# Kernel optimization log

Measured on AMD Instinct MI355X. Metric: run time of the kernel, lower is better.

## Reference

```python
import jax, jax.numpy as jnp
import numpy as np

N = 100000   # nodes
E = 3200000  # edges per graph
D = 16       # embedding_size, num_heads = 1
ATTN_SLOPE = 0.2   # DGL GATv2Conv negative_slope default
ACT_SLOPE = 0.01   # torch.nn.functional.leaky_relu default (activation arg)


def gatv2_layer(h, src, dst, W_src, b_src, W_dst, b_dst, attn):
    """DGL GATv2Conv with num_heads=1, activation=leaky_relu.
    h: [N, D]; src/dst: [E] int; W_*: [D, D]; b_*: [D]; attn: [D].
    """
    feat_src = h @ W_src + b_src          # [N, D]
    feat_dst = h @ W_dst + b_dst          # [N, D]
    el = feat_src[src]                    # [E, D] gather to edges
    e = jax.nn.leaky_relu(el + feat_dst[dst], ATTN_SLOPE)  # [E, D]
    score = e @ attn                      # [E] attention logits
    # segment softmax over incoming edges of each destination node
    smax = jax.ops.segment_max(score, dst, num_segments=N)
    smax = jnp.where(jnp.isfinite(smax), smax, 0.0)  # empty segments -> 0
    ex = jnp.exp(score - smax[dst])       # [E]
    denom = jax.ops.segment_sum(ex, dst, num_segments=N)  # [N]
    alpha = ex / denom[dst]               # [E]
    rst = jax.ops.segment_sum(alpha[:, None] * el, dst, num_segments=N)  # [N, D]
    return jax.nn.leaky_relu(rst, ACT_SLOPE)


def setup_inputs() -> dict:
    key = jax.random.key(0)
    ks = jax.random.split(key, 16)
    s = 1.0 / np.sqrt(D)
    return {
        "embedding": jax.random.normal(ks[0], (N, D), jnp.float32),
        "src1": jax.random.randint(ks[1], (E,), 0, N, jnp.int32),
        "dst1": jax.random.randint(ks[2], (E,), 0, N, jnp.int32),
        "src2": jax.random.randint(ks[3], (E,), 0, N, jnp.int32),
        "dst2": jax.random.randint(ks[4], (E,), 0, N, jnp.int32),
        "W_src1": jax.random.normal(ks[5], (D, D), jnp.float32) * s,
        "b_src1": jnp.zeros((D,), jnp.float32),
        "W_dst1": jax.random.normal(ks[6], (D, D), jnp.float32) * s,
        "b_dst1": jnp.zeros((D,), jnp.float32),
        "attn1": jax.random.normal(ks[7], (D,), jnp.float32) * s,
        "W_src2": jax.random.normal(ks[8], (D, D), jnp.float32) * s,
        "b_src2": jnp.zeros((D,), jnp.float32),
        "W_dst2": jax.random.normal(ks[9], (D, D), jnp.float32) * s,
        "b_dst2": jnp.zeros((D,), jnp.float32),
        "attn2": jax.random.normal(ks[10], (D,), jnp.float32) * s,
    }


def reference(embedding, src1, dst1, src2, dst2,
              W_src1, b_src1, W_dst1, b_dst1, attn1,
              W_src2, b_src2, W_dst2, b_dst2, attn2):
    user2item = gatv2_layer(embedding, src1, dst1, W_src1, b_src1, W_dst1, b_dst1, attn1)
    item_influence = gatv2_layer(user2item, src2, dst2, W_src2, b_src2, W_dst2, b_dst2, attn2)
    return item_influence  # [N, D]
```

## Files before the change

kernel.cpp:

```cpp
#include <hip/hip_runtime.h>
#include <hip/hip_fp16.h>

#define D 16
#define R 64
#define RBITS 6
#define RMASK 63
#define STRIDE 2560
#define CAP 2560
#define KPT (CAP / 256)
#define EPB 8192
#define SBT 1024
#define NBMAX 2048
#define ATTN_SLOPE 0.2f
#define ACT_SLOPE 0.01f

__device__ __forceinline__ float leaky_a(float v) {
    return v > 0.f ? v : ATTN_SLOPE * v;
}

__device__ __forceinline__ float2 h2f(unsigned u) {
    __half2 h = *(__half2*)&u;
    return __half22float2(h);
}

__device__ __forceinline__ int block_scan_pair(int pair, int tid, int* swsum) {
    int lane = tid & 63, w = tid >> 6;
    int x = pair;
#pragma unroll
    for (int ofs = 1; ofs < 64; ofs <<= 1) {
        int y = __shfl_up(x, ofs, 64);
        if (lane >= ofs) x += y;
    }
    if (lane == 63) swsum[w] = x;
    __syncthreads();
    if (w == 0) {
        int v = (lane < 16) ? swsum[lane] : 0;
        int s = v;
#pragma unroll
        for (int ofs = 1; ofs < 16; ofs <<= 1) {
            int y = __shfl_up(s, ofs, 64);
            if (lane >= ofs) s += y;
        }
        if (lane < 16) swsum[lane] = s - v;
    }
    __syncthreads();
    return x - pair + swsum[w];
}

__global__ void node_transform_kernel(const float* __restrict__ h,
                                      const float* __restrict__ Wsrc,
                                      const float* __restrict__ bsrc,
                                      const float* __restrict__ Wdst,
                                      const float* __restrict__ bdst,
                                      __half* __restrict__ feat_src_h,
                                      float* __restrict__ feat_dst,
                                      int* __restrict__ gcur,
                                      int N, int NB) {
    __shared__ float sWs[D * D], sWd[D * D], sbs[D], sbd[D];
    int t = threadIdx.x;
    if (t < D * D) {
        sWs[t] = Wsrc[t];
        sWd[t] = Wdst[t];
    }
    if (t < D) {
        sbs[t] = bsrc[t];
        sbd[t] = bdst[t];
    }
    int n = blockIdx.x * blockDim.x + t;
    if (n < NB) gcur[n] = n * STRIDE;
    __syncthreads();
    if (n >= N) return;
    float hv[D];
    const float4* h4 = (const float4*)(h + (size_t)n * D);
#pragma unroll
    for (int k = 0; k < 4; k++) {
        float4 v = h4[k];
        hv[4 * k] = v.x; hv[4 * k + 1] = v.y; hv[4 * k + 2] = v.z; hv[4 * k + 3] = v.w;
    }
    float os[D], od[D];
#pragma unroll
    for (int d = 0; d < D; d++) {
        float ss = sbs[d];
        float sd = sbd[d];
#pragma unroll
        for (int k = 0; k < D; k++) {
            ss += hv[k] * sWs[k * D + d];
            sd += hv[k] * sWd[k * D + d];
        }
        os[d] = ss; od[d] = sd;
    }
    unsigned us[8];
#pragma unroll
    for (int k = 0; k < 8; k++) {
        __half2 hh = __floats2half2_rn(os[2 * k], os[2 * k + 1]);
        us[k] = *(unsigned*)&hh;
    }
    uint4* fo = (uint4*)(feat_src_h + (size_t)n * D);
    fo[0] = make_uint4(us[0], us[1], us[2], us[3]);
    fo[1] = make_uint4(us[4], us[5], us[6], us[7]);
    float4* fd4 = (float4*)(feat_dst + (size_t)n * D);
#pragma unroll
    for (int k = 0; k < 4; k++)
        fd4[k] = make_float4(od[4 * k], od[4 * k + 1], od[4 * k + 2], od[4 * k + 3]);
}

__global__ void binscatter_kernel(const int* __restrict__ src, const int* __restrict__ dst,
                                  int* __restrict__ gcur, unsigned* __restrict__ binned,
                                  int E, int NB) {
    __shared__ unsigned sorted[EPB];
    __shared__ unsigned short sposb[EPB];
    __shared__ int shist[NBMAX];
    __shared__ int soffs[NBMAX];
    __shared__ int sgbase[NBMAX];
    __shared__ int swsum[16];
    int tid = threadIdx.x;
    int base = blockIdx.x * EPB;
    int count = E - base;
    if (count > EPB) count = EPB;

    for (int i = tid; i < NB; i += SBT) shist[i] = 0;
    __syncthreads();
    if (base + EPB <= E) {
        const int4* d4 = (const int4*)(dst + base);
#pragma unroll
        for (int k = 0; k < EPB / SBT / 4; k++) {
            int4 v = d4[k * SBT + tid];
            atomicAdd(&shist[v.x >> RBITS], 1);
            atomicAdd(&shist[v.y >> RBITS], 1);
            atomicAdd(&shist[v.z >> RBITS], 1);
            atomicAdd(&shist[v.w >> RBITS], 1);
        }
    } else {
#pragma unroll
        for (int k = 0; k < EPB / SBT; k++) {
            int e = base + k * SBT + tid;
            if (e < E) atomicAdd(&shist[dst[e] >> RBITS], 1);
        }
    }
    __syncthreads();
    int i0 = 2 * tid, i1 = 2 * tid + 1;
    int a0 = (i0 < NB) ? shist[i0] : 0;
    int a1 = (i1 < NB) ? shist[i1] : 0;
    int excl = block_scan_pair(a0 + a1, tid, swsum);
    if (i0 < NB) {
        shist[i0] = excl;
        soffs[i0] = excl;
        if (a0 > 0) sgbase[i0] = atomicAdd(&gcur[i0], a0);
    }
    if (i1 < NB) {
        shist[i1] = excl + a0;
        soffs[i1] = excl + a0;
        if (a1 > 0) sgbase[i1] = atomicAdd(&gcur[i1], a1);
    }
    __syncthreads();
    if (base + EPB <= E) {
        const int4* s4 = (const int4*)(src + base);
        const int4* d4 = (const int4*)(dst + base);
#pragma unroll
        for (int k = 0; k < EPB / SBT / 4; k++) {
            int4 sv = s4[k * SBT + tid];
            int4 dv = d4[k * SBT + tid];
            int ss[4] = {sv.x, sv.y, sv.z, sv.w};
            int dd[4] = {dv.x, dv.y, dv.z, dv.w};
#pragma unroll
            for (int m = 0; m < 4; m++) {
                int b = dd[m] >> RBITS;
                int r = atomicAdd(&soffs[b], 1);
                sorted[r] = ((unsigned)ss[m] << RBITS) | (unsigned)(dd[m] & RMASK);
                sposb[r] = (unsigned short)b;
            }
        }
    } else {
#pragma unroll
        for (int k = 0; k < EPB / SBT; k++) {
            int e = base + k * SBT + tid;
            if (e < E) {
                int dv = dst[e];
                int b = dv >> RBITS;
                int r = atomicAdd(&soffs[b], 1);
                sorted[r] = ((unsigned)src[e] << RBITS) | (unsigned)(dv & RMASK);
                sposb[r] = (unsigned short)b;
            }
        }
    }
    __syncthreads();
#pragma unroll
    for (int k = 0; k < EPB / SBT; k++) {
        int p = k * SBT + tid;
        if (p < count) {
            int bb = sposb[p];
            int pos = sgbase[bb] + (p - shist[bb]);
            if (pos < (bb + 1) * STRIDE) binned[pos] = sorted[p];
        }
    }
}

__global__ void __launch_bounds__(256)
accumulate_kernel(const unsigned* __restrict__ binned,
                  const int* __restrict__ gcur,
                  const __half* __restrict__ feat_src_h,
                  const float* __restrict__ feat_dst,
                  const float* __restrict__ attn,
                  float* __restrict__ out, int N) {
    __shared__ float sfd[R * D];
    __shared__ int ebuf[CAP];
    __shared__ float exbuf[CAP];
    __shared__ int cstart[R + 1];
    __shared__ int cur[R];
    int b = blockIdx.x;
    int tid = threadIdx.x;
    int node0 = b * R;
    int nn = N - node0;
    if (nn > R) nn = R;
    for (int i = tid; i < nn * D; i += 256) sfd[i] = feat_dst[node0 * D + i];
    if (tid <= R) cstart[tid] = 0;

    float av[D];
#pragma unroll
    for (int k = 0; k < D; k++) av[k] = attn[k];

    int base = b * STRIDE;
    int cnt = gcur[b] - base;
    if (cnt > CAP) cnt = CAP;

    unsigned pls[KPT];
#pragma unroll
    for (int k = 0; k < KPT; k++) {
        int j = k * 256 + tid;
        pls[k] = (j < cnt) ? binned[base + j] : 0xFFFFFFFFu;
    }
    __syncthreads();

    const uint4* fsh4 = (const uint4*)feat_src_h;
    const uint2* fsq = (const uint2*)feat_src_h;
    const float4* sfd4 = (const float4*)sfd;

#pragma unroll
    for (int k = 0; k < KPT; k++)
        if (pls[k] != 0xFFFFFFFFu) atomicAdd(&cstart[pls[k] & RMASK], 1);

    float exs[KPT];
#pragma unroll
    for (int k = 0; k < KPT; k += 2) {
        unsigned q0 = pls[k], q1 = pls[k + 1];
        uint4 ua0, ub0, ua1, ub1;
        if (q0 != 0xFFFFFFFFu) {
            int s = q0 >> RBITS;
            ua0 = fsh4[2 * s]; ub0 = fsh4[2 * s + 1];
        }
        if (q1 != 0xFFFFFFFFu) {
            int s = q1 >> RBITS;
            ua1 = fsh4[2 * s]; ub1 = fsh4[2 * s + 1];
        }
        if (q0 != 0xFFFFFFFFu) {
            int loc = q0 & RMASK;
            float4 f0 = sfd4[loc * 4 + 0], f1 = sfd4[loc * 4 + 1];
            float4 f2 = sfd4[loc * 4 + 2], f3 = sfd4[loc * 4 + 3];
            float2 c0 = h2f(ua0.x), c1 = h2f(ua0.y), c2 = h2f(ua0.z), c3 = h2f(ua0.w);
            float2 c4 = h2f(ub0.x), c5 = h2f(ub0.y), c6 = h2f(ub0.z), c7 = h2f(ub0.w);
            float p = leaky_a(c0.x + f0.x) * av[0]  + leaky_a(c0.y + f0.y) * av[1]
                    + leaky_a(c1.x + f0.z) * av[2]  + leaky_a(c1.y + f0.w) * av[3]
                    + leaky_a(c2.x + f1.x) * av[4]  + leaky_a(c2.y + f1.y) * av[5]
                    + leaky_a(c3.x + f1.z) * av[6]  + leaky_a(c3.y + f1.w) * av[7]
                    + leaky_a(c4.x + f2.x) * av[8]  + leaky_a(c4.y + f2.y) * av[9]
                    + leaky_a(c5.x + f2.z) * av[10] + leaky_a(c5.y + f2.w) * av[11]
                    + leaky_a(c6.x + f3.x) * av[12] + leaky_a(c6.y + f3.y) * av[13]
                    + leaky_a(c7.x + f3.z) * av[14] + leaky_a(c7.y + f3.w) * av[15];
            exs[k] = __expf(p);
        }
        if (q1 != 0xFFFFFFFFu) {
            int loc = q1 & RMASK;
            float4 f0 = sfd4[loc * 4 + 0], f1 = sfd4[loc * 4 + 1];
            float4 f2 = sfd4[loc * 4 + 2], f3 = sfd4[loc * 4 + 3];
            float2 c0 = h2f(ua1.x), c1 = h2f(ua1.y), c2 = h2f(ua1.z), c3 = h2f(ua1.w);
            float2 c4 = h2f(ub1.x), c5 = h2f(ub1.y), c6 = h2f(ub1.z), c7 = h2f(ub1.w);
            float p = leaky_a(c0.x + f0.x) * av[0]  + leaky_a(c0.y + f0.y) * av[1]
                    + leaky_a(c1.x + f0.z) * av[2]  + leaky_a(c1.y + f0.w) * av[3]
                    + leaky_a(c2.x + f1.x) * av[4]  + leaky_a(c2.y + f1.y) * av[5]
                    + leaky_a(c3.x + f1.z) * av[6]  + leaky_a(c3.y + f1.w) * av[7]
                    + leaky_a(c4.x + f2.x) * av[8]  + leaky_a(c4.y + f2.y) * av[9]
                    + leaky_a(c5.x + f2.z) * av[10] + leaky_a(c5.y + f2.w) * av[11]
                    + leaky_a(c6.x + f3.x) * av[12] + leaky_a(c6.y + f3.y) * av[13]
                    + leaky_a(c7.x + f3.z) * av[14] + leaky_a(c7.y + f3.w) * av[15];
            exs[k + 1] = __expf(p);
        }
    }
    __syncthreads();
    if (tid < R) {
        int v = cstart[tid];
        int x = v;
#pragma unroll
        for (int ofs = 1; ofs < 64; ofs <<= 1) {
            int y = __shfl_up(x, ofs, 64);
            if (tid >= ofs) x += y;
        }
        cstart[tid] = x - v;
        cur[tid] = x - v;
        if (tid == R - 1) cstart[R] = x;
    }
    __syncthreads();
#pragma unroll
    for (int k = 0; k < KPT; k++) {
        unsigned pl = pls[k];
        if (pl != 0xFFFFFFFFu) {
            int r = atomicAdd(&cur[pl & RMASK], 1);
            ebuf[r] = (int)pl;
            exbuf[r] = exs[k];
        }
    }
    __syncthreads();

    int lane = tid & 63;
    int w = tid >> 6;
    int q = lane & 3;
    int s2 = (lane >> 2) & 3;
    int n2 = lane >> 4;

    float4 acc[4];
    float den[4];
#pragma unroll
    for (int i = 0; i < 4; i++) {
        acc[i] = make_float4(0.f, 0.f, 0.f, 0.f);
        den[i] = 0.f;
    }
#pragma unroll
    for (int i = 0; i < 4; i++) {
        int loc = w * 16 + i * 4 + n2;
        int kb = cstart[loc], ke = cstart[loc + 1];
        int k = kb + s2;
        for (; k + 12 < ke; k += 16) {
            int pl0 = ebuf[k];
            int pl1 = ebuf[k + 4];
            int pl2 = ebuf[k + 8];
            int pl3 = ebuf[k + 12];
            float ex0 = exbuf[k];
            float ex1 = exbuf[k + 4];
            float ex2 = exbuf[k + 8];
            float ex3 = exbuf[k + 12];
            uint2 u0 = fsq[(((unsigned)pl0) >> RBITS) * 4 + q];
            uint2 u1 = fsq[(((unsigned)pl1) >> RBITS) * 4 + q];
            uint2 u2 = fsq[(((unsigned)pl2) >> RBITS) * 4 + q];
            uint2 u3 = fsq[(((unsigned)pl3) >> RBITS) * 4 + q];
            float2 a01 = h2f(u0.x), a23 = h2f(u0.y);
            float2 b01 = h2f(u1.x), b23 = h2f(u1.y);
            float2 c01 = h2f(u2.x), c23 = h2f(u2.y);
            float2 d01 = h2f(u3.x), d23 = h2f(u3.y);
            acc[i].x += ex0 * a01.x + ex1 * b01.x + ex2 * c01.x + ex3 * d01.x;
            acc[i].y += ex0 * a01.y + ex1 * b01.y + ex2 * c01.y + ex3 * d01.y;
            acc[i].z += ex0 * a23.x + ex1 * b23.x + ex2 * c23.x + ex3 * d23.x;
            acc[i].w += ex0 * a23.y + ex1 * b23.y + ex2 * c23.y + ex3 * d23.y;
            den[i] += (ex0 + ex1) + (ex2 + ex3);
        }
        for (; k < ke; k += 4) {
            int pl = ebuf[k];
            float ex = exbuf[k];
            uint2 u = fsq[(((unsigned)pl) >> RBITS) * 4 + q];
            float2 a01 = h2f(u.x), a23 = h2f(u.y);
            acc[i].x += ex * a01.x;
            acc[i].y += ex * a01.y;
            acc[i].z += ex * a23.x;
            acc[i].w += ex * a23.y;
            den[i] += ex;
        }
    }
#pragma unroll
    for (int i = 0; i < 4; i++) {
        float4 a = acc[i];
        float dn = den[i];
#pragma unroll
        for (int m = 4; m <= 8; m <<= 1) {
            a.x += __shfl_xor(a.x, m, 16);
            a.y += __shfl_xor(a.y, m, 16);
            a.z += __shfl_xor(a.z, m, 16);
            a.w += __shfl_xor(a.w, m, 16);
            dn += __shfl_xor(dn, m, 16);
        }
        int loc = w * 16 + i * 4 + n2;
        if (s2 == 0 && loc < nn) {
            float inv = dn > 0.f ? 1.f / dn : 0.f;
            float4 v;
            v.x = a.x * inv; v.x = v.x > 0.f ? v.x : ACT_SLOPE * v.x;
            v.y = a.y * inv; v.y = v.y > 0.f ? v.y : ACT_SLOPE * v.y;
            v.z = a.z * inv; v.z = v.z > 0.f ? v.z : ACT_SLOPE * v.z;
            v.w = a.w * inv; v.w = v.w > 0.f ? v.w : ACT_SLOPE * v.w;
            ((float4*)out)[(size_t)(node0 + loc) * 4 + q] = v;
        }
    }
}

static void run_layer(const float* h, const int* src, const int* dst,
                      const float* Wsrc, const float* bsrc,
                      const float* Wdst, const float* bdst, const float* attn,
                      __half* feat_src_h, float* feat_dst,
                      int* gcur, unsigned* binned,
                      float* out, int N, int E, hipStream_t stream) {
    const int NB = (N + R - 1) / R;
    const int EB = (E + EPB - 1) / EPB;

    node_transform_kernel<<<(N + 255) / 256, 256, 0, stream>>>(
        h, Wsrc, bsrc, Wdst, bdst, feat_src_h, feat_dst, gcur, N, NB);

    binscatter_kernel<<<EB, SBT, 0, stream>>>(src, dst, gcur, binned, E, NB);

    accumulate_kernel<<<NB, 256, 0, stream>>>(
        binned, gcur, feat_src_h, feat_dst, attn, out, N);
}

extern "C" void kernel_launch(void* const* d_in, const int* in_sizes, int n_in,
                              void* d_out, int out_size, void* d_ws, size_t ws_size,
                              hipStream_t stream) {
    const float* emb = (const float*)d_in[0];
    const int* src1 = (const int*)d_in[1];
    const int* dst1 = (const int*)d_in[2];
    const int* src2 = (const int*)d_in[3];
    const int* dst2 = (const int*)d_in[4];
    const float* Wsrc1 = (const float*)d_in[5];
    const float* bsrc1 = (const float*)d_in[6];
    const float* Wdst1 = (const float*)d_in[7];
    const float* bdst1 = (const float*)d_in[8];
    const float* attn1 = (const float*)d_in[9];
    const float* Wsrc2 = (const float*)d_in[10];
    const float* bsrc2 = (const float*)d_in[11];
    const float* Wdst2 = (const float*)d_in[12];
    const float* bdst2 = (const float*)d_in[13];
    const float* attn2 = (const float*)d_in[14];

    const int N = in_sizes[0] / D;
    const int E1 = in_sizes[1];
    const int E2 = in_sizes[3];

    float* ws = (float*)d_ws;
    float* feat_dst = ws;
    float* h2 = feat_dst + (size_t)N * D;
    __half* feat_src_h = (__half*)(h2 + (size_t)N * D);
    int* gcur = (int*)(feat_src_h + (size_t)N * D);
    unsigned* binned = (unsigned*)(gcur + NBMAX);
    (void)ws_size; (void)n_in; (void)out_size;

    run_layer(emb, src1, dst1, Wsrc1, bsrc1, Wdst1, bdst1, attn1,
              feat_src_h, feat_dst, gcur, binned, h2, N, E1, stream);

    run_layer(h2, src2, dst2, Wsrc2, bsrc2, Wdst2, bdst2, attn2,
              feat_src_h, feat_dst, gcur, binned, (float*)d_out, N, E2, stream);
}
```

Measured before the change: 275.4 us.

## Fuse both GATv2 layers into one persistent cooperative kernel with grid syncs

```diff
diff --git a/kernel.cpp b/kernel.cpp
--- a/kernel.cpp
+++ b/kernel.cpp
@@ -1,5 +1,8 @@
 #include <hip/hip_runtime.h>
 #include <hip/hip_fp16.h>
+#include <hip/hip_cooperative_groups.h>
+
+namespace cg = cooperative_groups;
 
 #define D 16
 #define R 64
@@ -8,19 +11,445 @@
 #define STRIDE 2560
 #define CAP 2560
 #define KPT (CAP / 256)
+#define ATTN_SLOPE 0.2f
+#define ACT_SLOPE 0.01f
+
+#define EPB2 2048
+#define NBX 1600
+#define SBUF_BYTES 25152
+#define NUM_CU 256
+
 #define EPB 8192
 #define SBT 1024
 #define NBMAX 2048
-#define ATTN_SLOPE 0.2f
-#define ACT_SLOPE 0.01f
 
 __device__ __forceinline__ float leaky_a(float v) {
     return v > 0.f ? v : ATTN_SLOPE * v;
 }
-
 __device__ __forceinline__ float2 h2f(unsigned u) {
     __half2 h = *(__half2*)&u;
     return __half22float2(h);
+}
+
+
+struct FusedParams {
+    const float* emb;
+    const int *src1, *dst1, *src2, *dst2;
+    const float *Ws1, *bs1, *Wd1, *bd1, *at1;
+    const float *Ws2, *bs2, *Wd2, *bd2, *at2;
+    __half* fs1h; float* fd1;
+    __half* fs2h; float* fd2;
+    int* gA; int* gB;
+    unsigned* binned;
+    float* out;
+    int N, E1, E2, NB;
+};
+
+__device__ void transform_phase(const float* __restrict__ h,
+                                const float* __restrict__ Ws, const float* __restrict__ bs,
+                                const float* __restrict__ Wd, const float* __restrict__ bd,
+                                __half* __restrict__ fsh, float* __restrict__ fdst,
+                                int* __restrict__ gA, int* __restrict__ gB,
+                                int N, int NB, char* sbuf, int gtid, int gsize) {
+    float* wb = (float*)sbuf;
+    int tid = threadIdx.x;
+    wb[tid] = Ws[tid];
+    wb[256 + tid] = Wd[tid];
+    if (tid < 16) { wb[512 + tid] = bs[tid]; wb[528 + tid] = bd[tid]; }
+    __syncthreads();
+    for (int i = gtid; i < NB; i += gsize) { gA[i] = 0; gB[i] = 0; }
+    for (int n = gtid; n < N; n += gsize) {
+        const float4* h4 = (const float4*)(h + (size_t)n * D);
+        float hv[16];
+#pragma unroll
+        for (int k2 = 0; k2 < 4; k2++) {
+            float4 v = h4[k2];
+            hv[4 * k2] = v.x; hv[4 * k2 + 1] = v.y; hv[4 * k2 + 2] = v.z; hv[4 * k2 + 3] = v.w;
+        }
+        uint2* fo = (uint2*)(fsh + (size_t)n * D);
+        float4* fdo = (float4*)(fdst + (size_t)n * D);
+#pragma unroll
+        for (int q = 0; q < 4; q++) {
+            float s0 = wb[512 + 4 * q], s1 = wb[513 + 4 * q], s2 = wb[514 + 4 * q], s3 = wb[515 + 4 * q];
+            float d0 = wb[528 + 4 * q], d1 = wb[529 + 4 * q], d2 = wb[530 + 4 * q], d3 = wb[531 + 4 * q];
+#pragma unroll
+            for (int k = 0; k < 16; k++) {
+                float hk = hv[k];
+                const float* wr = &wb[k * 16 + 4 * q];
+                const float* wr2 = &wb[256 + k * 16 + 4 * q];
+                s0 += hk * wr[0]; s1 += hk * wr[1]; s2 += hk * wr[2]; s3 += hk * wr[3];
+                d0 += hk * wr2[0]; d1 += hk * wr2[1]; d2 += hk * wr2[2]; d3 += hk * wr2[3];
+            }
+            __half2 p0 = __floats2half2_rn(s0, s1), p1 = __floats2half2_rn(s2, s3);
+            fo[q] = make_uint2(*(unsigned*)&p0, *(unsigned*)&p1);
+            fdo[q] = make_float4(d0, d1, d2, d3);
+        }
+    }
+}
+
+__device__ void binscatter_phase(const int* __restrict__ src, const int* __restrict__ dst,
+                                 int* __restrict__ gcur, unsigned* __restrict__ binned,
+                                 int E, int NB, char* sbuf) {
+    unsigned* sorted = (unsigned*)sbuf;
+    unsigned short* sposb = (unsigned short*)(sbuf + 8192);
+    int* soffs = (int*)(sbuf + 12288);
+    int* delta = (int*)(sbuf + 12288 + 4 * NBX);
+    int* wsum = (int*)(sbuf + 12288 + 8 * NBX);
+    int tid = threadIdx.x;
+    int numTiles = (E + EPB2 - 1) / EPB2;
+    for (int tile = blockIdx.x; tile < numTiles; tile += gridDim.x) {
+        __syncthreads();
+        int base = tile * EPB2;
+        int count = E - base;
+        if (count > EPB2) count = EPB2;
+        for (int i = tid; i < NB; i += 256) soffs[i] = 0;
+        __syncthreads();
+        if (count == EPB2) {
+            const int4* d4 = (const int4*)(dst + base);
+            int4 a = d4[tid], b = d4[256 + tid];
+            atomicAdd(&soffs[a.x >> RBITS], 1); atomicAdd(&soffs[a.y >> RBITS], 1);
+            atomicAdd(&soffs[a.z >> RBITS], 1); atomicAdd(&soffs[a.w >> RBITS], 1);
+            atomicAdd(&soffs[b.x >> RBITS], 1); atomicAdd(&soffs[b.y >> RBITS], 1);
+            atomicAdd(&soffs[b.z >> RBITS], 1); atomicAdd(&soffs[b.w >> RBITS], 1);
+        } else {
+            for (int k = 0; k < 8; k++) {
+                int e = base + k * 256 + tid;
+                if (e < E) atomicAdd(&soffs[dst[e] >> RBITS], 1);
+            }
+        }
+        __syncthreads();
+        int c[8];
+        int tsum = 0;
+#pragma unroll
+        for (int m = 0; m < 8; m++) {
+            int i = tid * 8 + m;
+            c[m] = (i < NB) ? soffs[i] : 0;
+            tsum += c[m];
+        }
+        int lane = tid & 63, w = tid >> 6;
+        int x = tsum;
+#pragma unroll
+        for (int ofs = 1; ofs < 64; ofs <<= 1) {
+            int y = __shfl_up(x, ofs, 64);
+            if (lane >= ofs) x += y;
+        }
+        if (lane == 63) wsum[w] = x;
+        __syncthreads();
+        int wofs = 0;
+        if (w > 0) wofs += wsum[0];
+        if (w > 1) wofs += wsum[1];
+        if (w > 2) wofs += wsum[2];
+        int run = x - tsum + wofs;
+        __syncthreads();
+#pragma unroll
+        for (int m = 0; m < 8; m++) {
+            int i = tid * 8 + m;
+            if (i < NB) {
+                soffs[i] = run;
+                if (c[m] > 0) {
+                    int res = atomicAdd(&gcur[i], c[m]);
+                    delta[i] = i * STRIDE + res - run;
+                }
+                run += c[m];
+            }
+        }
+        __syncthreads();
+        if (count == EPB2) {
+            const int4* s4 = (const int4*)(src + base);
+            const int4* d4 = (const int4*)(dst + base);
+            int4 sa = s4[tid], sb = s4[256 + tid], da = d4[tid], db = d4[256 + tid];
+            int ssv[8] = {sa.x, sa.y, sa.z, sa.w, sb.x, sb.y, sb.z, sb.w};
+            int ddv[8] = {da.x, da.y, da.z, da.w, db.x, db.y, db.z, db.w};
+#pragma unroll
+            for (int m = 0; m < 8; m++) {
+                int b = ddv[m] >> RBITS;
+                int r = atomicAdd(&soffs[b], 1);
+                sorted[r] = ((unsigned)ssv[m] << RBITS) | (unsigned)(ddv[m] & RMASK);
+                sposb[r] = (unsigned short)b;
+            }
+        } else {
+            for (int k = 0; k < 8; k++) {
+                int e = base + k * 256 + tid;
+                if (e < E) {
+                    int dv = dst[e];
+                    int b = dv >> RBITS;
+                    int r = atomicAdd(&soffs[b], 1);
+                    sorted[r] = ((unsigned)src[e] << RBITS) | (unsigned)(dv & RMASK);
+                    sposb[r] = (unsigned short)b;
+                }
+            }
+        }
+        __syncthreads();
+#pragma unroll
+        for (int m = 0; m < 8; m++) {
+            int p = m * 256 + tid;
+            if (p < count) {
+                int b = sposb[p];
+                int pos = p + delta[b];
+                if (pos < (b + 1) * STRIDE) binned[pos] = sorted[p];
+            }
+        }
+    }
+}
+
+template <bool DO_TAIL>
+__device__ void accumulate_phase(const unsigned* __restrict__ binned,
+                                 const int* __restrict__ gcur,
+                                 const __half* __restrict__ fsh,
+                                 const float* __restrict__ fdst,
+                                 const float* __restrict__ attn,
+                                 float* __restrict__ out,
+                                 __half* __restrict__ fs2h, float* __restrict__ fd2,
+                                 const float* __restrict__ Ws2, const float* __restrict__ bs2,
+                                 const float* __restrict__ Wd2, const float* __restrict__ bd2,
+                                 int N, int NB, char* sbuf) {
+    float* sfd = (float*)sbuf;
+    int* ebuf = (int*)(sbuf + 4096);
+    float* exbuf = (float*)(sbuf + 14336);
+    int* cstart = (int*)(sbuf + 24576);
+    int* cur = (int*)(sbuf + 24836);
+    int tid = threadIdx.x;
+    float av[D];
+#pragma unroll
+    for (int k = 0; k < D; k++) av[k] = attn[k];
+
+    const uint4* fsh4 = (const uint4*)fsh;
+    const uint2* fsq = (const uint2*)fsh;
+    const float4* sfd4 = (const float4*)sfd;
+
+    int lane = tid & 63;
+    int w = tid >> 6;
+    int q = lane & 3;
+    int s2 = (lane >> 2) & 3;
+    int n2 = lane >> 4;
+
+    for (int b = blockIdx.x; b < NB; b += gridDim.x) {
+        __syncthreads();
+        int node0 = b * R;
+        int nn = N - node0;
+        if (nn > R) nn = R;
+        for (int i = tid; i < nn * D; i += 256) sfd[i] = fdst[node0 * D + i];
+        if (tid <= R) cstart[tid] = 0;
+
+        int cnt = gcur[b];
+        if (cnt > CAP) cnt = CAP;
+        int base = b * STRIDE;
+
+        unsigned pls[KPT];
+#pragma unroll
+        for (int k = 0; k < KPT; k++) {
+            int j = k * 256 + tid;
+            pls[k] = (j < cnt) ? binned[base + j] : 0xFFFFFFFFu;
+        }
+        __syncthreads();
+
+#pragma unroll
+        for (int k = 0; k < KPT; k++)
+            if (pls[k] != 0xFFFFFFFFu) atomicAdd(&cstart[pls[k] & RMASK], 1);
+
+        float exs[KPT];
+#pragma unroll
+        for (int k = 0; k < KPT; k += 2) {
+            unsigned q0 = pls[k], q1 = pls[k + 1];
+            uint4 ua0, ub0, ua1, ub1;
+            if (q0 != 0xFFFFFFFFu) {
+                int s = q0 >> RBITS;
+                ua0 = fsh4[2 * s]; ub0 = fsh4[2 * s + 1];
+            }
+            if (q1 != 0xFFFFFFFFu) {
+                int s = q1 >> RBITS;
+                ua1 = fsh4[2 * s]; ub1 = fsh4[2 * s + 1];
+            }
+            if (q0 != 0xFFFFFFFFu) {
+                int loc = q0 & RMASK;
+                float4 f0 = sfd4[loc * 4 + 0], f1 = sfd4[loc * 4 + 1];
+                float4 f2 = sfd4[loc * 4 + 2], f3 = sfd4[loc * 4 + 3];
+                float2 c0 = h2f(ua0.x), c1 = h2f(ua0.y), c2 = h2f(ua0.z), c3 = h2f(ua0.w);
+                float2 c4 = h2f(ub0.x), c5 = h2f(ub0.y), c6 = h2f(ub0.z), c7 = h2f(ub0.w);
+                float p = leaky_a(c0.x + f0.x) * av[0]  + leaky_a(c0.y + f0.y) * av[1]
+                        + leaky_a(c1.x + f0.z) * av[2]  + leaky_a(c1.y + f0.w) * av[3]
+                        + leaky_a(c2.x + f1.x) * av[4]  + leaky_a(c2.y + f1.y) * av[5]
+                        + leaky_a(c3.x + f1.z) * av[6]  + leaky_a(c3.y + f1.w) * av[7]
+                        + leaky_a(c4.x + f2.x) * av[8]  + leaky_a(c4.y + f2.y) * av[9]
+                        + leaky_a(c5.x + f2.z) * av[10] + leaky_a(c5.y + f2.w) * av[11]
+                        + leaky_a(c6.x + f3.x) * av[12] + leaky_a(c6.y + f3.y) * av[13]
+                        + leaky_a(c7.x + f3.z) * av[14] + leaky_a(c7.y + f3.w) * av[15];
+                exs[k] = __expf(p);
+            }
+            if (q1 != 0xFFFFFFFFu) {
+                int loc = q1 & RMASK;
+                float4 f0 = sfd4[loc * 4 + 0], f1 = sfd4[loc * 4 + 1];
+                float4 f2 = sfd4[loc * 4 + 2], f3 = sfd4[loc * 4 + 3];
+                float2 c0 = h2f(ua1.x), c1 = h2f(ua1.y), c2 = h2f(ua1.z), c3 = h2f(ua1.w);
+                float2 c4 = h2f(ub1.x), c5 = h2f(ub1.y), c6 = h2f(ub1.z), c7 = h2f(ub1.w);
+                float p = leaky_a(c0.x + f0.x) * av[0]  + leaky_a(c0.y + f0.y) * av[1]
+                        + leaky_a(c1.x + f0.z) * av[2]  + leaky_a(c1.y + f0.w) * av[3]
+                        + leaky_a(c2.x + f1.x) * av[4]  + leaky_a(c2.y + f1.y) * av[5]
+                        + leaky_a(c3.x + f1.z) * av[6]  + leaky_a(c3.y + f1.w) * av[7]
+                        + leaky_a(c4.x + f2.x) * av[8]  + leaky_a(c4.y + f2.y) * av[9]
+                        + leaky_a(c5.x + f2.z) * av[10] + leaky_a(c5.y + f2.w) * av[11]
+                        + leaky_a(c6.x + f3.x) * av[12] + leaky_a(c6.y + f3.y) * av[13]
+                        + leaky_a(c7.x + f3.z) * av[14] + leaky_a(c7.y + f3.w) * av[15];
+                exs[k + 1] = __expf(p);
+            }
+        }
+        __syncthreads();
+        if (tid < R) {
+            int v = cstart[tid];
+            int x = v;
+#pragma unroll
+            for (int ofs = 1; ofs < 64; ofs <<= 1) {
+                int y = __shfl_up(x, ofs, 64);
+                if (tid >= ofs) x += y;
+            }
+            cstart[tid] = x - v;
+            cur[tid] = x - v;
+            if (tid == R - 1) cstart[R] = x;
+        }
+        __syncthreads();
+#pragma unroll
+        for (int k = 0; k < KPT; k++) {
+            unsigned pl = pls[k];
+            if (pl != 0xFFFFFFFFu) {
+                int r = atomicAdd(&cur[pl & RMASK], 1);
+                ebuf[r] = (int)pl;
+                exbuf[r] = exs[k];
+            }
+        }
+        __syncthreads();
+
+        float4 acc[4];
+        float den[4];
+#pragma unroll
+        for (int i = 0; i < 4; i++) {
+            acc[i] = make_float4(0.f, 0.f, 0.f, 0.f);
+            den[i] = 0.f;
+        }
+#pragma unroll
+        for (int i = 0; i < 4; i++) {
+            int loc = w * 16 + i * 4 + n2;
+            int kb = cstart[loc], ke = cstart[loc + 1];
+            int k = kb + s2;
+            for (; k + 12 < ke; k += 16) {
+                int pl0 = ebuf[k];
+                int pl1 = ebuf[k + 4];
+                int pl2 = ebuf[k + 8];
+                int pl3 = ebuf[k + 12];
+                float ex0 = exbuf[k];
+                float ex1 = exbuf[k + 4];
+                float ex2 = exbuf[k + 8];
+                float ex3 = exbuf[k + 12];
+                uint2 u0 = fsq[(((unsigned)pl0) >> RBITS) * 4 + q];
+                uint2 u1 = fsq[(((unsigned)pl1) >> RBITS) * 4 + q];
+                uint2 u2 = fsq[(((unsigned)pl2) >> RBITS) * 4 + q];
+                uint2 u3 = fsq[(((unsigned)pl3) >> RBITS) * 4 + q];
+                float2 a01 = h2f(u0.x), a23 = h2f(u0.y);
+                float2 b01 = h2f(u1.x), b23 = h2f(u1.y);
+                float2 c01 = h2f(u2.x), c23 = h2f(u2.y);
+                float2 d01 = h2f(u3.x), d23 = h2f(u3.y);
+                acc[i].x += ex0 * a01.x + ex1 * b01.x + ex2 * c01.x + ex3 * d01.x;
+                acc[i].y += ex0 * a01.y + ex1 * b01.y + ex2 * c01.y + ex3 * d01.y;
+                acc[i].z += ex0 * a23.x + ex1 * b23.x + ex2 * c23.x + ex3 * d23.x;
+                acc[i].w += ex0 * a23.y + ex1 * b23.y + ex2 * c23.y + ex3 * d23.y;
+                den[i] += (ex0 + ex1) + (ex2 + ex3);
+            }
+            for (; k < ke; k += 4) {
+                int pl = ebuf[k];
+                float ex = exbuf[k];
+                uint2 u = fsq[(((unsigned)pl) >> RBITS) * 4 + q];
+                float2 a01 = h2f(u.x), a23 = h2f(u.y);
+                acc[i].x += ex * a01.x;
+                acc[i].y += ex * a01.y;
+                acc[i].z += ex * a23.x;
+                acc[i].w += ex * a23.y;
+                den[i] += ex;
+            }
+        }
+#pragma unroll
+        for (int i = 0; i < 4; i++) {
+            float4 a = acc[i];
+            float dn = den[i];
+#pragma unroll
+            for (int m = 4; m <= 8; m <<= 1) {
+                a.x += __shfl_xor(a.x, m, 16);
+                a.y += __shfl_xor(a.y, m, 16);
+                a.z += __shfl_xor(a.z, m, 16);
+                a.w += __shfl_xor(a.w, m, 16);
+                dn += __shfl_xor(dn, m, 16);
+            }
+            int loc = w * 16 + i * 4 + n2;
+            if (s2 == 0 && loc < nn) {
+                float inv = dn > 0.f ? 1.f / dn : 0.f;
+                float4 v;
+                v.x = a.x * inv; v.x = v.x > 0.f ? v.x : ACT_SLOPE * v.x;
+                v.y = a.y * inv; v.y = v.y > 0.f ? v.y : ACT_SLOPE * v.y;
+                v.z = a.z * inv; v.z = v.z > 0.f ? v.z : ACT_SLOPE * v.z;
+                v.w = a.w * inv; v.w = v.w > 0.f ? v.w : ACT_SLOPE * v.w;
+                if (DO_TAIL) {
+                    *(float4*)&sfd[loc * D + q * 4] = v;
+                } else {
+                    ((float4*)out)[(size_t)(node0 + loc) * 4 + q] = v;
+                }
+            }
+        }
+        if (DO_TAIL) {
+            __syncthreads();
+            float* wb = (float*)ebuf;
+            wb[tid] = Ws2[tid];
+            wb[256 + tid] = Wd2[tid];
+            if (tid < 16) { wb[512 + tid] = bs2[tid]; wb[528 + tid] = bd2[tid]; }
+            __syncthreads();
+            int loc = tid >> 2, qq = tid & 3;
+            if (loc < nn) {
+                float hvv[16];
+#pragma unroll
+                for (int k = 0; k < 16; k++) hvv[k] = sfd[loc * D + k];
+                float s0 = wb[512 + 4 * qq], s1 = wb[513 + 4 * qq], s2v = wb[514 + 4 * qq], s3 = wb[515 + 4 * qq];
+                float d0 = wb[528 + 4 * qq], d1 = wb[529 + 4 * qq], d2v = wb[530 + 4 * qq], d3 = wb[531 + 4 * qq];
+#pragma unroll
+                for (int k = 0; k < 16; k++) {
+                    float hk = hvv[k];
+                    const float* wr = &wb[k * 16 + 4 * qq];
+                    const float* wr2 = &wb[256 + k * 16 + 4 * qq];
+                    s0 += hk * wr[0]; s1 += hk * wr[1]; s2v += hk * wr[2]; s3 += hk * wr[3];
+                    d0 += hk * wr2[0]; d1 += hk * wr2[1]; d2v += hk * wr2[2]; d3 += hk * wr2[3];
+                }
+                __half2 p0 = __floats2half2_rn(s0, s1), p1 = __floats2half2_rn(s2v, s3);
+                *(uint2*)(fs2h + (size_t)(node0 + loc) * D + 4 * qq) =
+                    make_uint2(*(unsigned*)&p0, *(unsigned*)&p1);
+                *(float4*)(fd2 + (size_t)(node0 + loc) * D + 4 * qq) =
+                    make_float4(d0, d1, d2v, d3);
+            }
+        }
+    }
+}
+
+__global__ void __launch_bounds__(256)
+fused_kernel(FusedParams p) {
+    __shared__ __align__(16) char sbuf[SBUF_BYTES];
+    cg::grid_group grid = cg::this_grid();
+    int gtid = blockIdx.x * 256 + threadIdx.x;
+    int gsize = gridDim.x * 256;
+
+    transform_phase(p.emb, p.Ws1, p.bs1, p.Wd1, p.bd1, p.fs1h, p.fd1,
+                    p.gA, p.gB, p.N, p.NB, sbuf, gtid, gsize);
+    grid.sync();
+    binscatter_phase(p.src1, p.dst1, p.gA, p.binned, p.E1, p.NB, sbuf);
+    grid.sync();
+    accumulate_phase<true>(p.binned, p.gA, p.fs1h, p.fd1, p.at1, nullptr,
+                           p.fs2h, p.fd2, p.Ws2, p.bs2, p.Wd2, p.bd2, p.N, p.NB, sbuf);
+    grid.sync();
+    binscatter_phase(p.src2, p.dst2, p.gB, p.binned, p.E2, p.NB, sbuf);
+    grid.sync();
+    accumulate_phase<false>(p.binned, p.gB, p.fs2h, p.fd2, p.at2, p.out,
+                            nullptr, nullptr, nullptr, nullptr, nullptr, nullptr,
+                            p.N, p.NB, sbuf);
+}
+
+
+__global__ void fixup_gcur_kernel(int* __restrict__ g, int nb) {
+    int i = blockIdx.x * blockDim.x + threadIdx.x;
+    if (i < nb) g[i] -= i * STRIDE;
 }
 
 __device__ __forceinline__ int block_scan_pair(int pair, int tid, int* swsum) {
@@ -120,22 +549,9 @@
 
     for (int i = tid; i < NB; i += SBT) shist[i] = 0;
     __syncthreads();
-    if (base + EPB <= E) {
-        const int4* d4 = (const int4*)(dst + base);
-#pragma unroll
-        for (int k = 0; k < EPB / SBT / 4; k++) {
-            int4 v = d4[k * SBT + tid];
-            atomicAdd(&shist[v.x >> RBITS], 1);
-            atomicAdd(&shist[v.y >> RBITS], 1);
-            atomicAdd(&shist[v.z >> RBITS], 1);
-            atomicAdd(&shist[v.w >> RBITS], 1);
-        }
-    } else {
-#pragma unroll
-        for (int k = 0; k < EPB / SBT; k++) {
-            int e = base + k * SBT + tid;
-            if (e < E) atomicAdd(&shist[dst[e] >> RBITS], 1);
-        }
+    for (int k = 0; k < EPB / SBT; k++) {
+        int e = base + k * SBT + tid;
+        if (e < E) atomicAdd(&shist[dst[e] >> RBITS], 1);
     }
     __syncthreads();
     int i0 = 2 * tid, i1 = 2 * tid + 1;
@@ -153,38 +569,17 @@
         if (a1 > 0) sgbase[i1] = atomicAdd(&gcur[i1], a1);
     }
     __syncthreads();
-    if (base + EPB <= E) {
-        const int4* s4 = (const int4*)(src + base);
-        const int4* d4 = (const int4*)(dst + base);
-#pragma unroll
-        for (int k = 0; k < EPB / SBT / 4; k++) {
-            int4 sv = s4[k * SBT + tid];
-            int4 dv = d4[k * SBT + tid];
-            int ss[4] = {sv.x, sv.y, sv.z, sv.w};
-            int dd[4] = {dv.x, dv.y, dv.z, dv.w};
-#pragma unroll
-            for (int m = 0; m < 4; m++) {
-                int b = dd[m] >> RBITS;
-                int r = atomicAdd(&soffs[b], 1);
-                sorted[r] = ((unsigned)ss[m] << RBITS) | (unsigned)(dd[m] & RMASK);
-                sposb[r] = (unsigned short)b;
-            }
-        }
-    } else {
-#pragma unroll
-        for (int k = 0; k < EPB / SBT; k++) {
-            int e = base + k * SBT + tid;
-            if (e < E) {
-                int dv = dst[e];
-                int b = dv >> RBITS;
-                int r = atomicAdd(&soffs[b], 1);
-                sorted[r] = ((unsigned)src[e] << RBITS) | (unsigned)(dv & RMASK);
-                sposb[r] = (unsigned short)b;
-            }
-        }
-    }
-    __syncthreads();
-#pragma unroll
+    for (int k = 0; k < EPB / SBT; k++) {
+        int e = base + k * SBT + tid;
+        if (e < E) {
+            int dv = dst[e];
+            int b = dv >> RBITS;
+            int r = atomicAdd(&soffs[b], 1);
+            sorted[r] = ((unsigned)src[e] << RBITS) | (unsigned)(dv & RMASK);
+            sposb[r] = (unsigned short)b;
+        }
+    }
+    __syncthreads();
     for (int k = 0; k < EPB / SBT; k++) {
         int p = k * SBT + tid;
         if (p < count) {
@@ -202,209 +597,12 @@
                   const float* __restrict__ feat_dst,
                   const float* __restrict__ attn,
                   float* __restrict__ out, int N) {
-    __shared__ float sfd[R * D];
-    __shared__ int ebuf[CAP];
-    __shared__ float exbuf[CAP];
-    __shared__ int cstart[R + 1];
-    __shared__ int cur[R];
-    int b = blockIdx.x;
-    int tid = threadIdx.x;
-    int node0 = b * R;
-    int nn = N - node0;
-    if (nn > R) nn = R;
-    for (int i = tid; i < nn * D; i += 256) sfd[i] = feat_dst[node0 * D + i];
-    if (tid <= R) cstart[tid] = 0;
-
-    float av[D];
-#pragma unroll
-    for (int k = 0; k < D; k++) av[k] = attn[k];
-
-    int base = b * STRIDE;
-    int cnt = gcur[b] - base;
-    if (cnt > CAP) cnt = CAP;
-
-    unsigned pls[KPT];
-#pragma unroll
-    for (int k = 0; k < KPT; k++) {
-        int j = k * 256 + tid;
-        pls[k] = (j < cnt) ? binned[base + j] : 0xFFFFFFFFu;
-    }
-    __syncthreads();
-
-    const uint4* fsh4 = (const uint4*)feat_src_h;
-    const uint2* fsq = (const uint2*)feat_src_h;
-    const float4* sfd4 = (const float4*)sfd;
-
-#pragma unroll
-    for (int k = 0; k < KPT; k++)
-        if (pls[k] != 0xFFFFFFFFu) atomicAdd(&cstart[pls[k] & RMASK], 1);
-
-    float exs[KPT];
-#pragma unroll
-    for (int k = 0; k < KPT; k += 2) {
-        unsigned q0 = pls[k], q1 = pls[k + 1];
-        uint4 ua0, ub0, ua1, ub1;
-        if (q0 != 0xFFFFFFFFu) {
-            int s = q0 >> RBITS;
-            ua0 = fsh4[2 * s]; ub0 = fsh4[2 * s + 1];
-        }
-        if (q1 != 0xFFFFFFFFu) {
-            int s = q1 >> RBITS;
-            ua1 = fsh4[2 * s]; ub1 = fsh4[2 * s + 1];
-        }
-        if (q0 != 0xFFFFFFFFu) {
-            int loc = q0 & RMASK;
-            float4 f0 = sfd4[loc * 4 + 0], f1 = sfd4[loc * 4 + 1];
-            float4 f2 = sfd4[loc * 4 + 2], f3 = sfd4[loc * 4 + 3];
-            float2 c0 = h2f(ua0.x), c1 = h2f(ua0.y), c2 = h2f(ua0.z), c3 = h2f(ua0.w);
-            float2 c4 = h2f(ub0.x), c5 = h2f(ub0.y), c6 = h2f(ub0.z), c7 = h2f(ub0.w);
-            float p = leaky_a(c0.x + f0.x) * av[0]  + leaky_a(c0.y + f0.y) * av[1]
-                    + leaky_a(c1.x + f0.z) * av[2]  + leaky_a(c1.y + f0.w) * av[3]
-                    + leaky_a(c2.x + f1.x) * av[4]  + leaky_a(c2.y + f1.y) * av[5]
-                    + leaky_a(c3.x + f1.z) * av[6]  + leaky_a(c3.y + f1.w) * av[7]
-                    + leaky_a(c4.x + f2.x) * av[8]  + leaky_a(c4.y + f2.y) * av[9]
-                    + leaky_a(c5.x + f2.z) * av[10] + leaky_a(c5.y + f2.w) * av[11]
-                    + leaky_a(c6.x + f3.x) * av[12] + leaky_a(c6.y + f3.y) * av[13]
-                    + leaky_a(c7.x + f3.z) * av[14] + leaky_a(c7.y + f3.w) * av[15];
-            exs[k] = __expf(p);
-        }
-        if (q1 != 0xFFFFFFFFu) {
-            int loc = q1 & RMASK;
-            float4 f0 = sfd4[loc * 4 + 0], f1 = sfd4[loc * 4 + 1];
-            float4 f2 = sfd4[loc * 4 + 2], f3 = sfd4[loc * 4 + 3];
-            float2 c0 = h2f(ua1.x), c1 = h2f(ua1.y), c2 = h2f(ua1.z), c3 = h2f(ua1.w);
-            float2 c4 = h2f(ub1.x), c5 = h2f(ub1.y), c6 = h2f(ub1.z), c7 = h2f(ub1.w);
-            float p = leaky_a(c0.x + f0.x) * av[0]  + leaky_a(c0.y + f0.y) * av[1]
-                    + leaky_a(c1.x + f0.z) * av[2]  + leaky_a(c1.y + f0.w) * av[3]
-                    + leaky_a(c2.x + f1.x) * av[4]  + leaky_a(c2.y + f1.y) * av[5]
-                    + leaky_a(c3.x + f1.z) * av[6]  + leaky_a(c3.y + f1.w) * av[7]
-                    + leaky_a(c4.x + f2.x) * av[8]  + leaky_a(c4.y + f2.y) * av[9]
-                    + leaky_a(c5.x + f2.z) * av[10] + leaky_a(c5.y + f2.w) * av[11]
-                    + leaky_a(c6.x + f3.x) * av[12] + leaky_a(c6.y + f3.y) * av[13]
-                    + leaky_a(c7.x + f3.z) * av[14] + leaky_a(c7.y + f3.w) * av[15];
-            exs[k + 1] = __expf(p);
-        }
-    }
-    __syncthreads();
-    if (tid < R) {
-        int v = cstart[tid];
-        int x = v;
-#pragma unroll
-        for (int ofs = 1; ofs < 64; ofs <<= 1) {
-            int y = __shfl_up(x, ofs, 64);
-            if (tid >= ofs) x += y;
-        }
-        cstart[tid] = x - v;
-        cur[tid] = x - v;
-        if (tid == R - 1) cstart[R] = x;
-    }
-    __syncthreads();
-#pragma unroll
-    for (int k = 0; k < KPT; k++) {
-        unsigned pl = pls[k];
-        if (pl != 0xFFFFFFFFu) {
-            int r = atomicAdd(&cur[pl & RMASK], 1);
-            ebuf[r] = (int)pl;
-            exbuf[r] = exs[k];
-        }
-    }
-    __syncthreads();
-
-    int lane = tid & 63;
-    int w = tid >> 6;
-    int q = lane & 3;
-    int s2 = (lane >> 2) & 3;
-    int n2 = lane >> 4;
-
-    float4 acc[4];
-    float den[4];
-#pragma unroll
-    for (int i = 0; i < 4; i++) {
-        acc[i] = make_float4(0.f, 0.f, 0.f, 0.f);
-        den[i] = 0.f;
-    }
-#pragma unroll
-    for (int i = 0; i < 4; i++) {
-        int loc = w * 16 + i * 4 + n2;
-        int kb = cstart[loc], ke = cstart[loc + 1];
-        int k = kb + s2;
-        for (; k + 12 < ke; k += 16) {
-            int pl0 = ebuf[k];
-            int pl1 = ebuf[k + 4];
-            int pl2 = ebuf[k + 8];
-            int pl3 = ebuf[k + 12];
-            float ex0 = exbuf[k];
-            float ex1 = exbuf[k + 4];
-            float ex2 = exbuf[k + 8];
-            float ex3 = exbuf[k + 12];
-            uint2 u0 = fsq[(((unsigned)pl0) >> RBITS) * 4 + q];
-            uint2 u1 = fsq[(((unsigned)pl1) >> RBITS) * 4 + q];
-            uint2 u2 = fsq[(((unsigned)pl2) >> RBITS) * 4 + q];
-            uint2 u3 = fsq[(((unsigned)pl3) >> RBITS) * 4 + q];
-            float2 a01 = h2f(u0.x), a23 = h2f(u0.y);
-            float2 b01 = h2f(u1.x), b23 = h2f(u1.y);
-            float2 c01 = h2f(u2.x), c23 = h2f(u2.y);
-            float2 d01 = h2f(u3.x), d23 = h2f(u3.y);
-            acc[i].x += ex0 * a01.x + ex1 * b01.x + ex2 * c01.x + ex3 * d01.x;
-            acc[i].y += ex0 * a01.y + ex1 * b01.y + ex2 * c01.y + ex3 * d01.y;
-            acc[i].z += ex0 * a23.x + ex1 * b23.x + ex2 * c23.x + ex3 * d23.x;
-            acc[i].w += ex0 * a23.y + ex1 * b23.y + ex2 * c23.y + ex3 * d23.y;
-            den[i] += (ex0 + ex1) + (ex2 + ex3);
-        }
-        for (; k < ke; k += 4) {
-            int pl = ebuf[k];
-            float ex = exbuf[k];
-            uint2 u = fsq[(((unsigned)pl) >> RBITS) * 4 + q];
-            float2 a01 = h2f(u.x), a23 = h2f(u.y);
-            acc[i].x += ex * a01.x;
-            acc[i].y += ex * a01.y;
-            acc[i].z += ex * a23.x;
-            acc[i].w += ex * a23.y;
-            den[i] += ex;
-        }
-    }
-#pragma unroll
-    for (int i = 0; i < 4; i++) {
-        float4 a = acc[i];
-        float dn = den[i];
-#pragma unroll
-        for (int m = 4; m <= 8; m <<= 1) {
-            a.x += __shfl_xor(a.x, m, 16);
-            a.y += __shfl_xor(a.y, m, 16);
-            a.z += __shfl_xor(a.z, m, 16);
-            a.w += __shfl_xor(a.w, m, 16);
-            dn += __shfl_xor(dn, m, 16);
-        }
-        int loc = w * 16 + i * 4 + n2;
-        if (s2 == 0 && loc < nn) {
-            float inv = dn > 0.f ? 1.f / dn : 0.f;
-            float4 v;
-            v.x = a.x * inv; v.x = v.x > 0.f ? v.x : ACT_SLOPE * v.x;
-            v.y = a.y * inv; v.y = v.y > 0.f ? v.y : ACT_SLOPE * v.y;
-            v.z = a.z * inv; v.z = v.z > 0.f ? v.z : ACT_SLOPE * v.z;
-            v.w = a.w * inv; v.w = v.w > 0.f ? v.w : ACT_SLOPE * v.w;
-            ((float4*)out)[(size_t)(node0 + loc) * 4 + q] = v;
-        }
-    }
-}
-
-static void run_layer(const float* h, const int* src, const int* dst,
-                      const float* Wsrc, const float* bsrc,
-                      const float* Wdst, const float* bdst, const float* attn,
-                      __half* feat_src_h, float* feat_dst,
-                      int* gcur, unsigned* binned,
-                      float* out, int N, int E, hipStream_t stream) {
-    const int NB = (N + R - 1) / R;
-    const int EB = (E + EPB - 1) / EPB;
-
-    node_transform_kernel<<<(N + 255) / 256, 256, 0, stream>>>(
-        h, Wsrc, bsrc, Wdst, bdst, feat_src_h, feat_dst, gcur, N, NB);
-
-    binscatter_kernel<<<EB, SBT, 0, stream>>>(src, dst, gcur, binned, E, NB);
-
-    accumulate_kernel<<<NB, 256, 0, stream>>>(
-        binned, gcur, feat_src_h, feat_dst, attn, out, N);
-}
+    __shared__ __align__(16) char sbuf[SBUF_BYTES];
+    accumulate_phase<false>(binned, gcur, feat_src_h, feat_dst, attn, out,
+                            nullptr, nullptr, nullptr, nullptr, nullptr, nullptr,
+                            N, gridDim.x, sbuf);
+}
+
 
 extern "C" void kernel_launch(void* const* d_in, const int* in_sizes, int n_in,
                               void* d_out, int out_size, void* d_ws, size_t ws_size,
@@ -428,18 +626,66 @@
     const int N = in_sizes[0] / D;
     const int E1 = in_sizes[1];
     const int E2 = in_sizes[3];
+    const int NB = (N + R - 1) / R;
 
     float* ws = (float*)d_ws;
-    float* feat_dst = ws;
-    float* h2 = feat_dst + (size_t)N * D;
-    __half* feat_src_h = (__half*)(h2 + (size_t)N * D);
-    int* gcur = (int*)(feat_src_h + (size_t)N * D);
-    unsigned* binned = (unsigned*)(gcur + NBMAX);
+    float* fd1 = ws;
+    float* fd2 = fd1 + (size_t)N * D;
+    __half* fs1h = (__half*)(fd2 + (size_t)N * D);
+    __half* fs2h = fs1h + (size_t)N * D;
+    int* gA = (int*)(fs2h + (size_t)N * D);
+    int* gB = gA + NBMAX;
+    unsigned* binned = (unsigned*)(gB + NBMAX);
     (void)ws_size; (void)n_in; (void)out_size;
 
-    run_layer(emb, src1, dst1, Wsrc1, bsrc1, Wdst1, bdst1, attn1,
-              feat_src_h, feat_dst, gcur, binned, h2, N, E1, stream);
-
-    run_layer(h2, src2, dst2, Wsrc2, bsrc2, Wdst2, bdst2, attn2,
-              feat_src_h, feat_dst, gcur, binned, (float*)d_out, N, E2, stream);
-}
+    int dev = 0;
+    (void)hipGetDevice(&dev);
+    int coop = 0;
+    (void)hipDeviceGetAttribute(&coop, hipDeviceAttributeCooperativeLaunch, dev);
+    int maxB = 0;
+    if (coop)
+        (void)hipOccupancyMaxActiveBlocksPerMultiprocessor(&maxB, fused_kernel, 256, 0);
+
+    if (coop && maxB > 0 && NB <= NBX) {
+        int nt1 = (E1 + EPB2 - 1) / EPB2;
+        int nt2 = (E2 + EPB2 - 1) / EPB2;
+        int needed = NB;
+        if (nt1 > needed) needed = nt1;
+        if (nt2 > needed) needed = nt2;
+        int ntr = (N + 255) / 256;
+        if (ntr > needed) needed = ntr;
+        int grid = maxB * NUM_CU;
+        if (grid > needed) grid = needed;
+
+        FusedParams prm;
+        prm.emb = emb;
+        prm.src1 = src1; prm.dst1 = dst1; prm.src2 = src2; prm.dst2 = dst2;
+        prm.Ws1 = Wsrc1; prm.bs1 = bsrc1; prm.Wd1 = Wdst1; prm.bd1 = bdst1; prm.at1 = attn1;
+        prm.Ws2 = Wsrc2; prm.bs2 = bsrc2; prm.Wd2 = Wdst2; prm.bd2 = bdst2; prm.at2 = attn2;
+        prm.fs1h = fs1h; prm.fd1 = fd1; prm.fs2h = fs2h; prm.fd2 = fd2;
+        prm.gA = gA; prm.gB = gB; prm.binned = binned; prm.out = (float*)d_out;
+        prm.N = N; prm.E1 = E1; prm.E2 = E2; prm.NB = NB;
+
+        void* args[] = {&prm};
+        (void)hipLaunchCooperativeKernel((void*)fused_kernel, dim3(grid), dim3(256),
+                                         args, 0, stream);
+    } else {
+        float* h2 = fd2;
+        const int EB1 = (E1 + EPB - 1) / EPB;
+        const int EB2 = (E2 + EPB - 1) / EPB;
+        const int NBG = (NB + 255) / 256;
+
+        node_transform_kernel<<<(N + 255) / 256, 256, 0, stream>>>(
+            emb, Wsrc1, bsrc1, Wdst1, bdst1, fs1h, fd1, gA, N, NB);
+        binscatter_kernel<<<EB1, SBT, 0, stream>>>(src1, dst1, gA, binned, E1, NB);
+        fixup_gcur_kernel<<<NBG, 256, 0, stream>>>(gA, NB);
+        accumulate_kernel<<<NB, 256, 0, stream>>>(binned, gA, fs1h, fd1, attn1, h2, N);
+
+        node_transform_kernel<<<(N + 255) / 256, 256, 0, stream>>>(
+            h2, Wsrc2, bsrc2, Wdst2, bdst2, fs1h, fd1, gB, N, NB);
+        binscatter_kernel<<<EB2, SBT, 0, stream>>>(src2, dst2, gB, binned, E2, NB);
+        fixup_gcur_kernel<<<NBG, 256, 0, stream>>>(gB, NB);
+        accumulate_kernel<<<NB, 256, 0, stream>>>(binned, gB, fs1h, fd1, attn2,
+                                                  (float*)d_out, N);
+    }
+}
```

Measured after the change: 435.3 us. 58.0% more time.
